# Kernel tuning notes

Hardware: AMD Instinct MI355X
Metric: run time of the kernel (lower is better)

Reference implementation:

```python
import jax, jax.numpy as jnp
import numpy as np

ALPHA = 2.0   # snntorch ATan surrogate default
THRESH = 1.0  # snntorch Leaky default threshold

@jax.custom_vjp
def spike(x):
    return (x > 0).astype(x.dtype)

def _spike_fwd(x):
    return spike(x), x

def _spike_bwd(x, g):
    # ATan surrogate gradient: (alpha/2) / (1 + (pi/2 * alpha * x)^2)
    return (g * (ALPHA / 2) / (1 + (jnp.pi / 2 * ALPHA * x) ** 2),)

spike.defvjp(_spike_fwd, _spike_bwd)

def _lif(inp, mem, beta):
    # snntorch Leaky, reset_mechanism='subtract':
    # reset from previous mem (detached), then integrate, then fire
    reset = jax.lax.stop_gradient(spike(mem - THRESH))
    mem = jnp.clip(beta, 0.0, 1.0) * mem + inp - reset * THRESH
    spk = spike(mem - THRESH)
    return spk, mem

def setup_inputs() -> dict:
    key = jax.random.key(0)
    ks = jax.random.split(key, 8)
    V, H, T, B = 32000, 512, 512, 8
    s = 0.02
    inv = 1.0 / np.sqrt(H)
    return {
        "x": jax.random.randint(ks[0], (T, B), 0, V),
        "emb": jax.random.normal(ks[1], (V, H), jnp.float32) * s,
        "pos_emb": jax.random.normal(ks[2], (T, H), jnp.float32) * s,
        "beta1": jnp.full((H,), 0.9, jnp.float32),
        "beta2": jnp.full((H,), 0.9, jnp.float32),
        "beta3": jnp.full((H,), 0.9, jnp.float32),
        "W2": jax.random.normal(ks[3], (H, H), jnp.float32) * inv,
        "b2": jnp.zeros((H,), jnp.float32),
        "W3": jax.random.normal(ks[4], (H, H), jnp.float32) * inv,
        "b3": jnp.zeros((H,), jnp.float32),
        "Wout": jax.random.normal(ks[5], (V, H), jnp.float32) * inv,
        "bout": jnp.zeros((V,), jnp.float32),
    }

def reference(x, emb, pos_emb, beta1, beta2, beta3, W2, b2, W3, b3, Wout, bout):
    T, B = x.shape
    H = emb.shape[1]
    # precompute token + positional embedding for all steps: [T, B, H]
    hid = emb[x] + pos_emb[:, None, :]
    mem0 = jnp.zeros((B, H), emb.dtype)

    def step(carry, h_t):
        m1, m2, m3 = carry
        spk1, m1 = _lif(h_t, m1, beta1)
        h = jax.nn.relu(spk1 @ W2.T + b2)
        spk2, m2 = _lif(h, m2, beta2)
        h = jax.nn.relu(spk2 @ W3.T + b3)
        spk3, m3 = _lif(h, m3, beta3)
        logits = spk3 @ Wout.T + bout  # [B, V]
        return (m1, m2, m3), logits

    _, out = jax.lax.scan(step, (mem0, mem0, mem0), hid)
    return out  # [T, B, V]
```

## Files before the change

kernel.cpp:

```cpp
#include <hip/hip_runtime.h>

#define TT 512
#define BB 8
#define HH 512
#define VV 32000
#define RR (TT * BB)

__device__ __forceinline__ float clip01(float x) { return fminf(fmaxf(x, 0.0f), 1.0f); }

__global__ void zero_cnt_kernel(int* __restrict__ cnt, int n) {
    int i = blockIdx.x * blockDim.x + threadIdx.x;
    if (i < n) cnt[i] = 0;
}

__global__ void lif1_kernel(const int* __restrict__ x, const float* __restrict__ emb,
                            const float* __restrict__ pos, const float* __restrict__ beta,
                            int* __restrict__ cnt, int* __restrict__ act) {
    __shared__ int x_lds[TT];
    int tid = blockIdx.x * 256 + threadIdx.x;
    int b = tid >> 9;
    int h = tid & (HH - 1);
    for (int t = threadIdx.x; t < TT; t += 256) x_lds[t] = x[t * BB + b];
    __syncthreads();
    float bt = clip01(beta[h]);
    float m = 0.0f;
    for (int t0 = 0; t0 < TT; t0 += 8) {
        float inp[8];
#pragma unroll
        for (int u = 0; u < 8; ++u) {
            int xv = x_lds[t0 + u];
            inp[u] = emb[xv * HH + h] + pos[(t0 + u) * HH + h];
        }
#pragma unroll
        for (int u = 0; u < 8; ++u) {
            float reset = (m > 1.0f) ? 1.0f : 0.0f;
            m = bt * m + inp[u] - reset;
            if (m > 1.0f) {
                int r = (t0 + u) * BB + b;
                int p = atomicAdd(&cnt[r], 1);
                act[(r << 9) + p] = h;
            }
        }
    }
}

__global__ void lif_scan_kernel(const float* __restrict__ Z, const float* __restrict__ beta,
                                int* __restrict__ cnt, int* __restrict__ act) {
    int tid = blockIdx.x * 256 + threadIdx.x;
    int b = tid >> 9;
    int h = tid & (HH - 1);
    float bt = clip01(beta[h]);
    float m = 0.0f;
    for (int t0 = 0; t0 < TT; t0 += 8) {
        float inp[8];
#pragma unroll
        for (int u = 0; u < 8; ++u) inp[u] = Z[(((t0 + u) * BB + b) << 9) + h];
#pragma unroll
        for (int u = 0; u < 8; ++u) {
            float reset = (m > 1.0f) ? 1.0f : 0.0f;
            m = bt * m + inp[u] - reset;
            if (m > 1.0f) {
                int r = (t0 + u) * BB + b;
                int p = atomicAdd(&cnt[r], 1);
                act[(r << 9) + p] = h;
            }
        }
    }
}

__global__ void sp_gemm_kernel(const int* __restrict__ cnt, const int* __restrict__ act,
                               const float* __restrict__ W, const float* __restrict__ bias,
                               float* __restrict__ Z) {
    int r = blockIdx.x;
    int j = threadIdx.x;
    int n = cnt[r];
    float acc = bias[j];
    const int* a = act + (r << 9);
    for (int i = 0; i < n; ++i) {
        int k = a[i];
        acc += W[(j << 9) + k];
    }
    Z[(r << 9) + j] = fmaxf(acc, 0.0f);
}

__global__ void out_gemm_kernel(const int* __restrict__ cnt, const int* __restrict__ act,
                                const float* __restrict__ Wout, const float* __restrict__ bout,
                                float* __restrict__ out) {
    int v = blockIdx.x * 2048 + threadIdx.x * 4;
    if (v >= VV) return;
    float4 bv = *(const float4*)(bout + v);
    int r0 = blockIdx.y * 8;
#pragma unroll
    for (int rr = 0; rr < 8; ++rr) {
        int r = r0 + rr;
        int n = cnt[r];
        float4 acc = bv;
        const int* a = act + (r << 9);
        for (int i = 0; i < n; ++i) {
            int k = a[i];
            acc.x += Wout[(v + 0) * HH + k];
            acc.y += Wout[(v + 1) * HH + k];
            acc.z += Wout[(v + 2) * HH + k];
            acc.w += Wout[(v + 3) * HH + k];
        }
        *(float4*)(out + (size_t)r * VV + v) = acc;
    }
}

extern "C" void kernel_launch(void* const* d_in, const int* in_sizes, int n_in,
                              void* d_out, int out_size, void* d_ws, size_t ws_size,
                              hipStream_t stream) {
    const int*   x     = (const int*)d_in[0];
    const float* emb   = (const float*)d_in[1];
    const float* pos   = (const float*)d_in[2];
    const float* beta1 = (const float*)d_in[3];
    const float* beta2 = (const float*)d_in[4];
    const float* beta3 = (const float*)d_in[5];
    const float* W2    = (const float*)d_in[6];
    const float* b2    = (const float*)d_in[7];
    const float* W3    = (const float*)d_in[8];
    const float* b3    = (const float*)d_in[9];
    const float* Wout  = (const float*)d_in[10];
    const float* bout  = (const float*)d_in[11];
    float* out = (float*)d_out;

    float* Z    = (float*)d_ws;
    int*   actA = (int*)(Z + (size_t)RR * HH);
    int*   actB = actA + (size_t)RR * HH;
    int*   cntA = actB + (size_t)RR * HH;
    int*   cntB = cntA + RR;
    int*   cntC = cntB + RR;

    zero_cnt_kernel<<<(3 * RR + 255) / 256, 256, 0, stream>>>(cntA, 3 * RR);
    lif1_kernel<<<16, 256, 0, stream>>>(x, emb, pos, beta1, cntA, actA);
    sp_gemm_kernel<<<RR, 512, 0, stream>>>(cntA, actA, W2, b2, Z);
    lif_scan_kernel<<<16, 256, 0, stream>>>(Z, beta2, cntB, actB);
    sp_gemm_kernel<<<RR, 512, 0, stream>>>(cntB, actB, W3, b3, Z);
    lif_scan_kernel<<<16, 256, 0, stream>>>(Z, beta3, cntC, actA);
    out_gemm_kernel<<<dim3(16, RR / 8), 512, 0, stream>>>(cntC, actA, Wout, bout, out);
}
```

Before: 722.3 us.

## Fuse sparse hidden GEMMs into LIF scans and precompute embedding gather

Adds a fully parallel gather kernel that builds token+position embeddings and zeroes the spike counters, replacing the separate zeroing kernel. The LIF1 scan then streams precomputed inputs. Each hidden sparse GEMM is folded into the following LIF scan: every thread accumulates its W row over the active spike list per timestep, so the dense Z intermediate and two launches disappear. The risk is that the serial scan now does the GEMM work on only 8 blocks, which is costly if spikes are dense, and the workspace needs one more activation buffer.

```diff
diff --git a/kernel.cpp b/kernel.cpp
--- a/kernel.cpp
+++ b/kernel.cpp
@@ -8,31 +8,31 @@
 
 __device__ __forceinline__ float clip01(float x) { return fminf(fmaxf(x, 0.0f), 1.0f); }
 
-__global__ void zero_cnt_kernel(int* __restrict__ cnt, int n) {
-    int i = blockIdx.x * blockDim.x + threadIdx.x;
-    if (i < n) cnt[i] = 0;
+__global__ void gather_kernel(const int* __restrict__ x, const float* __restrict__ emb,
+                              const float* __restrict__ pos, float* __restrict__ hid,
+                              int* __restrict__ cnt_all) {
+    int r = blockIdx.x;
+    int h = threadIdx.x;
+    int t = r >> 3;
+    int xv = x[r];
+    hid[((size_t)r << 9) + h] = emb[((size_t)xv << 9) + h] + pos[(t << 9) + h];
+    if (r < 3 * RR / HH)
+        cnt_all[(r << 9) + h] = 0;
 }
 
-__global__ void lif1_kernel(const int* __restrict__ x, const float* __restrict__ emb,
-                            const float* __restrict__ pos, const float* __restrict__ beta,
+__global__ void lif1_kernel(const float* __restrict__ hid, const float* __restrict__ beta,
                             int* __restrict__ cnt, int* __restrict__ act) {
-    __shared__ int x_lds[TT];
-    int tid = blockIdx.x * 256 + threadIdx.x;
-    int b = tid >> 9;
-    int h = tid & (HH - 1);
-    for (int t = threadIdx.x; t < TT; t += 256) x_lds[t] = x[t * BB + b];
-    __syncthreads();
+    int b = blockIdx.x;
+    int h = threadIdx.x;
+    const float* base = hid + ((size_t)b << 9) + h;
     float bt = clip01(beta[h]);
     float m = 0.0f;
-    for (int t0 = 0; t0 < TT; t0 += 8) {
-        float inp[8];
+    for (int t0 = 0; t0 < TT; t0 += 16) {
+        float inp[16];
 #pragma unroll
-        for (int u = 0; u < 8; ++u) {
-            int xv = x_lds[t0 + u];
-            inp[u] = emb[xv * HH + h] + pos[(t0 + u) * HH + h];
-        }
+        for (int u = 0; u < 16; ++u) inp[u] = base[(size_t)(t0 + u) * (BB * HH)];
 #pragma unroll
-        for (int u = 0; u < 8; ++u) {
+        for (int u = 0; u < 16; ++u) {
             float reset = (m > 1.0f) ? 1.0f : 0.0f;
             m = bt * m + inp[u] - reset;
             if (m > 1.0f) {
@@ -44,43 +44,43 @@
     }
 }
 
-__global__ void lif_scan_kernel(const float* __restrict__ Z, const float* __restrict__ beta,
-                                int* __restrict__ cnt, int* __restrict__ act) {
-    int tid = blockIdx.x * 256 + threadIdx.x;
-    int b = tid >> 9;
-    int h = tid & (HH - 1);
+__global__ void lif_fused_kernel(const int* __restrict__ cnt_in, const int* __restrict__ act_in,
+                                 const float* __restrict__ W, const float* __restrict__ bias,
+                                 const float* __restrict__ beta,
+                                 int* __restrict__ cnt_out, int* __restrict__ act_out) {
+    __shared__ int c[TT];
+    int b = blockIdx.x;
+    int h = threadIdx.x;
+    c[h] = cnt_in[h * BB + b];
+    __syncthreads();
+    float bh = bias[h];
+    float inp0 = fmaxf(bh, 0.0f);
     float bt = clip01(beta[h]);
     float m = 0.0f;
-    for (int t0 = 0; t0 < TT; t0 += 8) {
-        float inp[8];
+    for (int t0 = 0; t0 < TT; t0 += 16) {
+        int n[16];
 #pragma unroll
-        for (int u = 0; u < 8; ++u) inp[u] = Z[(((t0 + u) * BB + b) << 9) + h];
+        for (int u = 0; u < 16; ++u) n[u] = c[t0 + u];
 #pragma unroll
-        for (int u = 0; u < 8; ++u) {
+        for (int u = 0; u < 16; ++u) {
+            float inp;
+            if (n[u] == 0) {
+                inp = inp0;
+            } else {
+                float acc = bh;
+                const int* a = act_in + (((t0 + u) * BB + b) << 9);
+                for (int i = 0; i < n[u]; ++i) acc += W[(h << 9) + a[i]];
+                inp = fmaxf(acc, 0.0f);
+            }
             float reset = (m > 1.0f) ? 1.0f : 0.0f;
-            m = bt * m + inp[u] - reset;
+            m = bt * m + inp - reset;
             if (m > 1.0f) {
                 int r = (t0 + u) * BB + b;
-                int p = atomicAdd(&cnt[r], 1);
-                act[(r << 9) + p] = h;
+                int p = atomicAdd(&cnt_out[r], 1);
+                act_out[(r << 9) + p] = h;
             }
         }
     }
-}
-
-__global__ void sp_gemm_kernel(const int* __restrict__ cnt, const int* __restrict__ act,
-                               const float* __restrict__ W, const float* __restrict__ bias,
-                               float* __restrict__ Z) {
-    int r = blockIdx.x;
-    int j = threadIdx.x;
-    int n = cnt[r];
-    float acc = bias[j];
-    const int* a = act + (r << 9);
-    for (int i = 0; i < n; ++i) {
-        int k = a[i];
-        acc += W[(j << 9) + k];
-    }
-    Z[(r << 9) + j] = fmaxf(acc, 0.0f);
 }
 
 __global__ void out_gemm_kernel(const int* __restrict__ cnt, const int* __restrict__ act,
@@ -98,10 +98,10 @@
         const int* a = act + (r << 9);
         for (int i = 0; i < n; ++i) {
             int k = a[i];
-            acc.x += Wout[(v + 0) * HH + k];
-            acc.y += Wout[(v + 1) * HH + k];
-            acc.z += Wout[(v + 2) * HH + k];
-            acc.w += Wout[(v + 3) * HH + k];
+            acc.x += Wout[(size_t)(v + 0) * HH + k];
+            acc.y += Wout[(size_t)(v + 1) * HH + k];
+            acc.z += Wout[(size_t)(v + 2) * HH + k];
+            acc.w += Wout[(size_t)(v + 3) * HH + k];
         }
         *(float4*)(out + (size_t)r * VV + v) = acc;
     }
@@ -124,18 +124,17 @@
     const float* bout  = (const float*)d_in[11];
     float* out = (float*)d_out;
 
-    float* Z    = (float*)d_ws;
-    int*   actA = (int*)(Z + (size_t)RR * HH);
-    int*   actB = actA + (size_t)RR * HH;
-    int*   cntA = actB + (size_t)RR * HH;
-    int*   cntB = cntA + RR;
-    int*   cntC = cntB + RR;
+    float* hid  = (float*)d_ws;
+    int*   act1 = (int*)(hid + (size_t)RR * HH);
+    int*   act2 = act1 + (size_t)RR * HH;
+    int*   act3 = act2 + (size_t)RR * HH;
+    int*   cnt1 = act3 + (size_t)RR * HH;
+    int*   cnt2 = cnt1 + RR;
+    int*   cnt3 = cnt2 + RR;
 
-    zero_cnt_kernel<<<(3 * RR + 255) / 256, 256, 0, stream>>>(cntA, 3 * RR);
-    lif1_kernel<<<16, 256, 0, stream>>>(x, emb, pos, beta1, cntA, actA);
-    sp_gemm_kernel<<<RR, 512, 0, stream>>>(cntA, actA, W2, b2, Z);
-    lif_scan_kernel<<<16, 256, 0, stream>>>(Z, beta2, cntB, actB);
-    sp_gemm_kernel<<<RR, 512, 0, stream>>>(cntB, actB, W3, b3, Z);
-    lif_scan_kernel<<<16, 256, 0, stream>>>(Z, beta3, cntC, actA);
-    out_gemm_kernel<<<dim3(16, RR / 8), 512, 0, stream>>>(cntC, actA, Wout, bout, out);
+    gather_kernel<<<RR, HH, 0, stream>>>(x, emb, pos, hid, cnt1);
+    lif1_kernel<<<BB, HH, 0, stream>>>(hid, beta1, cnt1, act1);
+    lif_fused_kernel<<<BB, HH, 0, stream>>>(cnt1, act1, W2, b2, beta2, cnt2, act2);
+    lif_fused_kernel<<<BB, HH, 0, stream>>>(cnt2, act2, W3, b3, beta3, cnt3, act3);
+    out_gemm_kernel<<<dim3(16, RR / 8), HH, 0, stream>>>(cnt3, act3, Wout, bout, out);
 }
```

Result: faster. 681.9 us (-5.6%).
